# Optimization experiments

Hardware: AMD Instinct MI355X
Metric: run time of the kernel (lower is better)

## Reference

```python
import jax, jax.numpy as jnp
import numpy as np

VOCAB = 100000
EMB_DIM = 128
MAX_KP = 50  # config.max_num_keyphrases; lens tensors are constant-filled with this
EPS = 1e-8   # torch cosine_similarity eps


def setup_inputs() -> dict:
    key = jax.random.key(0)
    k1, k2, k3, k4 = jax.random.split(key, 4)
    B, A, K = 64, 32, 50
    batch_source = jax.random.randint(k1, (B, A, K), 0, VOCAB)
    pos_result = jax.random.randint(k2, (B, A, K), 0, VOCAB)
    neg_result = jax.random.randint(k3, (B, A, K), 0, VOCAB)
    emb_table = jax.random.normal(k4, (VOCAB + 1, EMB_DIM), dtype=jnp.float32)
    emb_table = emb_table.at[0].set(0.0)  # padding_idx=0
    return {
        "batch_source": batch_source,
        "pos_result": pos_result,
        "neg_result": neg_result,
        "emb_table": emb_table,
    }


def _embed(emb_table, idx):
    # idx: [B, A, K] -> mean-pooled [B, A, D]; denominator is the constant MAX_KP
    emb = emb_table[idx]                      # [B, A, K, D] gather (memory-bound)
    return jnp.sum(emb, axis=-2) / MAX_KP     # [B, A, D]


def _l2norm(x):
    n = jnp.sqrt(jnp.sum(x * x, axis=-1, keepdims=True))
    return x / jnp.maximum(n, EPS)


def _max_cosine(src_e, tgt_e):
    # src_e: [B, A1, D], tgt_e: [B, A2, D] -> max over all (A1, A2) pairs, per batch
    sims = jnp.einsum("bad,bcd->bac", _l2norm(src_e), _l2norm(tgt_e))  # [B, A1, A2]
    return jnp.max(sims, axis=(1, 2))  # [B]


def reference(batch_source, pos_result, neg_result, emb_table):
    src_e = _embed(emb_table, batch_source)
    pos_e = _embed(emb_table, pos_result)
    neg_e = _embed(emb_table, neg_result)
    pos_scores = _max_cosine(src_e, pos_e)  # [B]
    neg_scores = _max_cosine(src_e, neg_e)  # [B]
    x = pos_scores - neg_scores
    # BCEWithLogitsLoss with target = 1: mean(softplus(-x))
    loss = jnp.mean(jax.nn.softplus(-x))
    return loss
```

## Files before the change

### kernel.cpp

```cpp
#include <hip/hip_runtime.h>
#include <math.h>

#define BB 64
#define AA 32
#define KK 50
#define DD 128
#define MAX_KP 50
#define EPS_CS 1e-8f
#define NVEC (3 * BB * AA)

__device__ __forceinline__ float dot4(float4 a, float4 b) {
    return a.x * b.x + a.y * b.y + a.z * b.z + a.w * b.w;
}

__global__ __launch_bounds__(128) void embed_norm_kernel(
    const int* __restrict__ src, const int* __restrict__ pos,
    const int* __restrict__ neg, const float* __restrict__ table,
    float* __restrict__ out)
{
    const int vec = __builtin_amdgcn_readfirstlane(
        (blockIdx.x << 1) | (threadIdx.x >> 6));
    const int t  = vec >> 11;
    const int ba = vec & 2047;
    const int* idx = ((t == 0) ? src : (t == 1) ? pos : neg) + ba * KK;

    const int lane = threadIdx.x & 63;
    const int half = lane >> 5;
    const int slot = lane & 31;

    const float4* tab4 = (const float4*)table;
    float4 acc = make_float4(0.f, 0.f, 0.f, 0.f);
    #pragma unroll
    for (int i = 0; i < KK / 2; ++i) {
        const int r0 = idx[2 * i];
        const int r1 = idx[2 * i + 1];
        const int row = half ? r1 : r0;
        const float4 v = tab4[(row << 5) + slot];
        acc.x += v.x; acc.y += v.y; acc.z += v.z; acc.w += v.w;
    }

    acc.x += __shfl_xor(acc.x, 32, 64);
    acc.y += __shfl_xor(acc.y, 32, 64);
    acc.z += __shfl_xor(acc.z, 32, 64);
    acc.w += __shfl_xor(acc.w, 32, 64);

    const float s = 1.0f / MAX_KP;
    acc.x *= s; acc.y *= s; acc.z *= s; acc.w *= s;

    float sq = dot4(acc, acc);
    #pragma unroll
    for (int off = 16; off > 0; off >>= 1) sq += __shfl_xor(sq, off, 64);

    const float inv = 1.0f / fmaxf(sqrtf(sq), EPS_CS);
    acc.x *= inv; acc.y *= inv; acc.z *= inv; acc.w *= inv;

    if (lane < 32)
        ((float4*)out)[(vec << 5) + slot] = acc;
}

__global__ __launch_bounds__(256) void cosine_part_kernel(
    const float* __restrict__ embs, float* __restrict__ part )
{
    const int blk = blockIdx.x;
    const int b   = blk >> 2;
    const int q   = blk & 3;
    const int tens  = q >> 1;
    const int ihalf = q & 1;
    const int tid = threadIdx.x;

    __shared__ float s_src[16][DD + 4];
    __shared__ float s_tgt[AA][DD + 4];

    const float4* src4 = (const float4*)(embs + ((long)b * AA + ihalf * 16) * DD);
    const float4* tgt4 = (const float4*)(embs + (long)(BB + tens * BB + b) * AA * DD);

    for (int i = tid; i < 16 * DD / 4; i += 256) {
        const int r = i >> 5, c = i & 31;
        *(float4*)&s_src[r][c * 4] = src4[i];
    }
    for (int i = tid; i < AA * DD / 4; i += 256) {
        const int r = i >> 5, c = i & 31;
        *(float4*)&s_tgt[r][c * 4] = tgt4[i];
    }
    __syncthreads();

    const int si = tid >> 4;
    const int j  = tid & 15;

    float d0s = 0.f, d1s = 0.f;
    #pragma unroll 8
    for (int d0 = 0; d0 < DD; d0 += 4) {
        const float4 a  = *(const float4*)&s_src[si][d0];
        const float4 t0 = *(const float4*)&s_tgt[j][d0];
        const float4 t1 = *(const float4*)&s_tgt[j + 16][d0];
        d0s += dot4(a, t0);
        d1s += dot4(a, t1);
    }
    float m = fmaxf(d0s, d1s);

    #pragma unroll
    for (int off = 32; off > 0; off >>= 1) m = fmaxf(m, __shfl_xor(m, off, 64));
    __shared__ float sm[4];
    if ((tid & 63) == 0) sm[tid >> 6] = m;
    __syncthreads();

    if (tid == 0)
        part[blk] = fmaxf(fmaxf(sm[0], sm[1]), fmaxf(sm[2], sm[3]));
}

__global__ void finalize_kernel(const float* __restrict__ part,
                                float* __restrict__ out)
{
    const int b = threadIdx.x;
    const float P = fmaxf(part[b * 4 + 0], part[b * 4 + 1]);
    const float N = fmaxf(part[b * 4 + 2], part[b * 4 + 3]);
    const float x = P - N;
    float l = (x >= 0.f) ? log1pf(expf(-x)) : (-x + log1pf(expf(x)));
    #pragma unroll
    for (int off = 32; off > 0; off >>= 1) l += __shfl_xor(l, off, 64);
    if (b == 0) out[0] = l * (1.0f / BB);
}

extern "C" void kernel_launch(void* const* d_in, const int* in_sizes, int n_in,
                              void* d_out, int out_size, void* d_ws, size_t ws_size,
                              hipStream_t stream) {
    const int*   batch_source = (const int*)d_in[0];
    const int*   pos_result   = (const int*)d_in[1];
    const int*   neg_result   = (const int*)d_in[2];
    const float* emb_table    = (const float*)d_in[3];
    float* out = (float*)d_out;

    float* embs = (float*)d_ws;
    float* part = embs + 3L * BB * AA * DD;

    embed_norm_kernel<<<NVEC / 2, 128, 0, stream>>>(
        batch_source, pos_result, neg_result, emb_table, embs);
    cosine_part_kernel<<<4 * BB, 256, 0, stream>>>(embs, part);
    finalize_kernel<<<1, 64, 0, stream>>>(part, out);
}
```

Before: 34.37 us.

## Fuse finalize into cosine kernel via last-block atomic counter; split target halves

Removes the separate finalize launch. The last cosine block to finish, detected with an agent-scope atomic counter, computes the softplus loss. The counter is reset at the start of the embed kernel. The cosine grid is doubled to 512 blocks, each handling a 16x16 tile instead of 16x32, which adds parallelism and cuts shared memory per block. The cost is the atomics plus the serial tail work done in a single block.

```diff
diff --git a/kernel.cpp b/kernel.cpp
--- a/kernel.cpp
+++ b/kernel.cpp
@@ -8,6 +8,7 @@
 #define MAX_KP 50
 #define EPS_CS 1e-8f
 #define NVEC (3 * BB * AA)
+#define NCOS (8 * BB)
 
 __device__ __forceinline__ float dot4(float4 a, float4 b) {
     return a.x * b.x + a.y * b.y + a.z * b.z + a.w * b.w;
@@ -16,8 +17,10 @@
 __global__ __launch_bounds__(128) void embed_norm_kernel(
     const int* __restrict__ src, const int* __restrict__ pos,
     const int* __restrict__ neg, const float* __restrict__ table,
-    float* __restrict__ out)
+    float* __restrict__ out, unsigned* __restrict__ cnt)
 {
+    if (blockIdx.x == 0 && threadIdx.x == 0) cnt[0] = 0u;
+
     const int vec = __builtin_amdgcn_readfirstlane(
         (blockIdx.x << 1) | (threadIdx.x >> 6));
     const int t  = vec >> 11;
@@ -58,28 +61,28 @@
         ((float4*)out)[(vec << 5) + slot] = acc;
 }
 
-__global__ __launch_bounds__(256) void cosine_part_kernel(
-    const float* __restrict__ embs, float* __restrict__ part )
+__global__ __launch_bounds__(256) void cosine_loss_kernel(
+    const float* __restrict__ embs, float* __restrict__ part ,
+    unsigned* __restrict__ cnt, float* __restrict__ out)
 {
-    const int blk = blockIdx.x;
-    const int b   = blk >> 2;
-    const int q   = blk & 3;
-    const int tens  = q >> 1;
-    const int ihalf = q & 1;
-    const int tid = threadIdx.x;
+    const int blk  = blockIdx.x;
+    const int b    = blk >> 3;
+    const int q    = blk & 7;
+    const int tens = q >> 2;
+    const int ih   = (q >> 1) & 1;
+    const int jh   = q & 1;
+    const int tid  = threadIdx.x;
 
     __shared__ float s_src[16][DD + 4];
-    __shared__ float s_tgt[AA][DD + 4];
+    __shared__ float s_tgt[16][DD + 4];
 
-    const float4* src4 = (const float4*)(embs + ((long)b * AA + ihalf * 16) * DD);
-    const float4* tgt4 = (const float4*)(embs + (long)(BB + tens * BB + b) * AA * DD);
+    const float4* src4 = (const float4*)(embs + ((long)b * AA + ih * 16) * DD);
+    const float4* tgt4 = (const float4*)(embs +
+                          ((long)(BB + tens * BB + b) * AA + jh * 16) * DD);
 
     for (int i = tid; i < 16 * DD / 4; i += 256) {
         const int r = i >> 5, c = i & 31;
         *(float4*)&s_src[r][c * 4] = src4[i];
-    }
-    for (int i = tid; i < AA * DD / 4; i += 256) {
-        const int r = i >> 5, c = i & 31;
         *(float4*)&s_tgt[r][c * 4] = tgt4[i];
     }
     __syncthreads();
@@ -87,38 +90,47 @@
     const int si = tid >> 4;
     const int j  = tid & 15;
 
-    float d0s = 0.f, d1s = 0.f;
+    float dsum = 0.f;
     #pragma unroll 8
-    for (int d0 = 0; d0 < DD; d0 += 4) {
-        const float4 a  = *(const float4*)&s_src[si][d0];
-        const float4 t0 = *(const float4*)&s_tgt[j][d0];
-        const float4 t1 = *(const float4*)&s_tgt[j + 16][d0];
-        d0s += dot4(a, t0);
-        d1s += dot4(a, t1);
-    }
-    float m = fmaxf(d0s, d1s);
+    for (int d0 = 0; d0 < DD; d0 += 4)
+        dsum += dot4(*(const float4*)&s_src[si][d0],
+                     *(const float4*)&s_tgt[j][d0]);
 
+    float m = dsum;
     #pragma unroll
     for (int off = 32; off > 0; off >>= 1) m = fmaxf(m, __shfl_xor(m, off, 64));
     __shared__ float sm[4];
+    __shared__ int s_win;
     if ((tid & 63) == 0) sm[tid >> 6] = m;
     __syncthreads();
 
-    if (tid == 0)
-        part[blk] = fmaxf(fmaxf(sm[0], sm[1]), fmaxf(sm[2], sm[3]));
-}
+    if (tid == 0) {
+        const float bm = fmaxf(fmaxf(sm[0], sm[1]), fmaxf(sm[2], sm[3]));
+        __hip_atomic_store(&part[blk], bm, __ATOMIC_RELAXED,
+                           __HIP_MEMORY_SCOPE_AGENT);
+        const unsigned old = __hip_atomic_fetch_add(
+            cnt, 1u, __ATOMIC_ACQ_REL, __HIP_MEMORY_SCOPE_AGENT);
+        s_win = (old == NCOS - 1);
+    }
+    __syncthreads();
+    if (!s_win) return;
 
-__global__ void finalize_kernel(const float* __restrict__ part,
-                                float* __restrict__ out)
-{
-    const int b = threadIdx.x;
-    const float P = fmaxf(part[b * 4 + 0], part[b * 4 + 1]);
-    const float N = fmaxf(part[b * 4 + 2], part[b * 4 + 3]);
-    const float x = P - N;
-    float l = (x >= 0.f) ? log1pf(expf(-x)) : (-x + log1pf(expf(x)));
-    #pragma unroll
-    for (int off = 32; off > 0; off >>= 1) l += __shfl_xor(l, off, 64);
-    if (b == 0) out[0] = l * (1.0f / BB);
+    if (tid < BB) {
+        float v[8];
+        v[0] = __hip_atomic_load(&part[tid * 8 + 0], __ATOMIC_ACQUIRE,
+                                 __HIP_MEMORY_SCOPE_AGENT);
+        #pragma unroll
+        for (int k = 1; k < 8; ++k)
+            v[k] = __hip_atomic_load(&part[tid * 8 + k], __ATOMIC_RELAXED,
+                                     __HIP_MEMORY_SCOPE_AGENT);
+        const float P = fmaxf(fmaxf(v[0], v[1]), fmaxf(v[2], v[3]));
+        const float N = fmaxf(fmaxf(v[4], v[5]), fmaxf(v[6], v[7]));
+        const float x = P - N;
+        float l = (x >= 0.f) ? log1pf(expf(-x)) : (-x + log1pf(expf(x)));
+        #pragma unroll
+        for (int off = 32; off > 0; off >>= 1) l += __shfl_xor(l, off, 64);
+        if (tid == 0) out[0] = l * (1.0f / BB);
+    }
 }
 
 extern "C" void kernel_launch(void* const* d_in, const int* in_sizes, int n_in,
@@ -130,11 +142,11 @@
     const float* emb_table    = (const float*)d_in[3];
     float* out = (float*)d_out;
 
-    float* embs = (float*)d_ws;
-    float* part = embs + 3L * BB * AA * DD;
+    float*    embs = (float*)d_ws;
+    float*    part = embs + 3L * BB * AA * DD;
+    unsigned* cnt  = (unsigned*)(part + NCOS);
 
     embed_norm_kernel<<<NVEC / 2, 128, 0, stream>>>(
-        batch_source, pos_result, neg_result, emb_table, embs);
-    cosine_part_kernel<<<4 * BB, 256, 0, stream>>>(embs, part);
-    finalize_kernel<<<1, 64, 0, stream>>>(part, out);
+        batch_source, pos_result, neg_result, emb_table, embs, cnt);
+    cosine_loss_kernel<<<NCOS, 256, 0, stream>>>(embs, part, cnt, out);
 }
```

Result: slower. 40.44 us (+17.6%).
